# Performance work log

Measured on AMD Instinct MI355X. Metric: run time of the kernel, lower is better.

## Reference

```python
import jax, jax.numpy as jnp
import numpy as np

B, P, M = 2, 2048, 1024
H, D = 16, 64  # num_heads, head_dim; M == H*D

def setup_inputs() -> dict:
    key = jax.random.key(0)
    k1, k2, k3 = jax.random.split(key, 3)
    x = jax.random.normal(k1, (B, P, M), dtype=jnp.float32)
    W_attn = jax.random.normal(k2, (M, 3 * M), dtype=jnp.float32) * 0.02
    b_attn = jnp.zeros((3 * M,), dtype=jnp.float32)
    W_proj = jax.random.normal(k3, (M, M), dtype=jnp.float32) * 0.02
    b_proj = jnp.zeros((M,), dtype=jnp.float32)
    return {"x": x, "W_attn": W_attn, "b_attn": b_attn, "W_proj": W_proj, "b_proj": b_proj}

def reference(x, W_attn, b_attn, W_proj, b_proj):
    b, p, m = x.shape
    # fused QKV projection
    qkv = jnp.einsum('bpm,mn->bpn', x, W_attn) + b_attn  # [b,p,3m]
    q, k, v = jnp.split(qkv, 3, axis=2)
    q = q.reshape(b, p, H, D)
    k = k.reshape(b, p, H, D)
    v = v.reshape(b, p, H, D)
    q = q / jnp.sqrt(jnp.asarray(D, dtype=q.dtype))
    scores = jnp.einsum('bqhd,bkhd->bhqk', q, k)  # [b,h,p,p]
    causal = jnp.tril(jnp.ones((p, p), dtype=bool))  # [p,p]
    big_neg = jnp.finfo(jnp.float32).min
    scores = jnp.where(causal[None, None, :, :], scores, big_neg)
    pattern = jax.nn.softmax(scores, axis=-1)
    z = jnp.einsum('bhqk,bkhd->bqhd', pattern, v)  # [b,p,h,d]
    z = z.reshape(b, p, m)
    out = jnp.einsum('bpm,mn->bpn', z, W_proj) + b_proj
    return out
```

## Files before the change

### kernel.cpp

```cpp
#include <hip/hip_runtime.h>
#include <hip/hip_bf16.h>

typedef __bf16 bf16;
typedef __attribute__((ext_vector_type(8))) __bf16 bf16x8;
typedef __attribute__((ext_vector_type(4))) float f32x4;

#define MFMA16(a, b, c) __builtin_amdgcn_mfma_f32_16x16x32_bf16(a, b, c, 0, 0, 0)
#define GLL16(gp, lp)                                                          \
  __builtin_amdgcn_global_load_lds(                                            \
      (const __attribute__((address_space(1))) void*)(gp),                     \
      (__attribute__((address_space(3))) void*)(lp), 16, 0, 0)

constexpr int Bsz = 2, Pseq = 2048, Mdim = 1024, NH = 16, Dh = 64;
constexpr int ROWS = Bsz * Pseq;
constexpr float LOG2E = 1.4426950408889634f;
constexpr float BIG_NEG = -3.0e38f;
constexpr float M0 = 8.0f;

__global__ __launch_bounds__(256) void k_pre(const float* __restrict__ X,
                                             bf16* __restrict__ Xb,
                                             const float* __restrict__ Wa,
                                             bf16* __restrict__ Wat,
                                             const float* __restrict__ Wp,
                                             bf16* __restrict__ Wpt) {
  __shared__ __align__(16) bf16 tile[64][72];
  int blk = blockIdx.x;
  int t = threadIdx.x;
  if (blk < 1024) {
    const f32x4* X4 = (const f32x4*)X;
    int i0 = blk * 1024 + t;
#pragma unroll
    for (int c = 0; c < 4; ++c) {
      int i = i0 + c * 256;
      f32x4 v = X4[i];
      union { bf16 h[4]; uint2 u; } pk;
      pk.h[0] = (bf16)v[0]; pk.h[1] = (bf16)v[1];
      pk.h[2] = (bf16)v[2]; pk.h[3] = (bf16)v[3];
      ((uint2*)Xb)[i] = pk.u;
    }
    return;
  }
  const float* W; bf16* Wt; int Ndim, n0, k0;
  if (blk < 1792) {
    int bx = blk - 1024;
    W = Wa; Wt = Wat; Ndim = 3 * Mdim;
    n0 = (bx % 48) * 64; k0 = (bx / 48) * 64;
  } else {
    int bx = blk - 1792;
    W = Wp; Wt = Wpt; Ndim = Mdim;
    n0 = (bx & 15) * 64; k0 = (bx >> 4) * 64;
  }
  int tc = t & 15, tr = t >> 4;
#pragma unroll
  for (int pass = 0; pass < 4; ++pass) {
    int r = tr + pass * 16;
    f32x4 v = *(const f32x4*)(W + (size_t)(k0 + r) * Ndim + n0 + tc * 4);
#pragma unroll
    for (int i = 0; i < 4; ++i) tile[tc * 4 + i][r] = (bf16)v[i];
  }
  __syncthreads();
#pragma unroll
  for (int pass = 0; pass < 4; ++pass) {
    int n = tr + pass * 16;
    union { bf16 h[4]; uint2 u; } pk;
#pragma unroll
    for (int i = 0; i < 4; ++i) pk.h[i] = tile[n][tc * 4 + i];
    *(uint2*)(Wt + (size_t)(n0 + n) * Mdim + k0 + tc * 4) = pk.u;
  }
}

template <int TM, int TN>
__device__ __forceinline__ void gemm_core(const bf16* __restrict__ A,
                                          const bf16* __restrict__ Bt,
                                          bf16* Ash, bf16* Bsh, int K,
                                          int row0, int col0,
                                          f32x4 (&acc)[TM / 32][TN / 32]) {
  constexpr int MT = TM / 32, NT = TN / 32;
  int tid = threadIdx.x;
  int lane = tid & 63, w = tid >> 6;
  int l15 = lane & 15, g = lane >> 4, l7 = lane & 7, l8 = lane >> 3;
  int wm = w & 1, wn = w >> 1;
  const bf16* Ag = A + (size_t)(row0 + w * 8 + l8) * K + (l7 ^ l8) * 8;
  const bf16* Bg = Bt + (size_t)(col0 + w * 8 + l8) * K + (l7 ^ l8) * 8;
  bf16* Asb = Ash + w * 512;
  bf16* Bsb = Bsh + w * 512;
  for (int k0 = 0; k0 < K; k0 += 64) {
#pragma unroll
    for (int p = 0; p < MT; ++p)
      GLL16(Ag + (size_t)(p * 32) * K + k0, Asb + p * 2048);
#pragma unroll
    for (int p = 0; p < NT; ++p)
      GLL16(Bg + (size_t)(p * 32) * K + k0, Bsb + p * 2048);
    __syncthreads();
#pragma unroll
    for (int ks = 0; ks < 2; ++ks) {
      int swz = ((ks * 4 + g) ^ l7) * 8;
      bf16x8 af[MT], bfr[NT];
#pragma unroll
      for (int mt = 0; mt < MT; ++mt)
        af[mt] = *(const bf16x8*)(Ash + (wm * (TM / 2) + mt * 16 + l15) * 64 + swz);
#pragma unroll
      for (int nt = 0; nt < NT; ++nt)
        bfr[nt] = *(const bf16x8*)(Bsh + (wn * (TN / 2) + nt * 16 + l15) * 64 + swz);
#pragma unroll
      for (int mt = 0; mt < MT; ++mt)
#pragma unroll
        for (int nt = 0; nt < NT; ++nt)
          acc[mt][nt] = MFMA16(af[mt], bfr[nt], acc[mt][nt]);
    }
    __syncthreads();
  }
}

__global__ __launch_bounds__(512) void k_qkv(const bf16* __restrict__ Xb,
                                             const bf16* __restrict__ Wt,
                                             const float* __restrict__ bias,
                                             bf16* __restrict__ Qo,
                                             bf16* __restrict__ Ko,
                                             bf16* __restrict__ Vto) {
  __shared__ __align__(16) bf16 Ash[128 * 64], Bsh[128 * 64];
  int cb = blockIdx.x, rb = blockIdx.y;
  int row0 = rb * 128, col0 = cb * 128;
  int tid = threadIdx.x;
  int lane = tid & 63, w = tid >> 6;
  int l15 = lane & 15, g = lane >> 4, l7 = lane & 7;
  int wm = w & 1, wn = w >> 1;
  int sr = tid >> 3;
  int sc = (tid & 7) ^ (sr & 7);
  const bf16* Ag = Xb + (size_t)(row0 + sr) * Mdim + sc * 8;
  const bf16* Bg = Wt + (size_t)(col0 + sr) * Mdim + sc * 8;

  f32x4 acc[4][2];
  const f32x4 zero = {0.f, 0.f, 0.f, 0.f};
#pragma unroll
  for (int mt = 0; mt < 4; ++mt)
#pragma unroll
    for (int nt = 0; nt < 2; ++nt) acc[mt][nt] = zero;

  for (int k0 = 0; k0 < Mdim; k0 += 64) {
    GLL16(Ag + k0, Ash + tid * 8);
    GLL16(Ag + (size_t)64 * Mdim + k0, Ash + 4096 + tid * 8);
    GLL16(Bg + k0, Bsh + tid * 8);
    GLL16(Bg + (size_t)64 * Mdim + k0, Bsh + 4096 + tid * 8);
    __syncthreads();
#pragma unroll
    for (int ks = 0; ks < 2; ++ks) {
      int swz = ((ks * 4 + g) ^ l7) * 8;
      bf16x8 af[4], bfr[2];
#pragma unroll
      for (int mt = 0; mt < 4; ++mt)
        af[mt] = *(const bf16x8*)(Ash + (wm * 64 + mt * 16 + l15) * 64 + swz);
#pragma unroll
      for (int nt = 0; nt < 2; ++nt)
        bfr[nt] = *(const bf16x8*)(Bsh + (wn * 32 + nt * 16 + l15) * 64 + swz);
#pragma unroll
      for (int mt = 0; mt < 4; ++mt)
#pragma unroll
        for (int nt = 0; nt < 2; ++nt)
          acc[mt][nt] = MFMA16(af[mt], bfr[nt], acc[mt][nt]);
    }
    __syncthreads();
  }

  int sec = cb >> 3;
  if (sec < 2) {
    bf16* out = sec == 0 ? Qo : Ko;
    float scale = sec == 0 ? (0.125f * LOG2E) : 1.0f;
#pragma unroll
    for (int nt = 0; nt < 2; ++nt) {
      int col = col0 + wn * 32 + nt * 16 + l15;
      int cm = col & 1023;
      int h = cm >> 6, d = cm & 63;
      float bv = bias[col];
#pragma unroll
      for (int mt = 0; mt < 4; ++mt)
#pragma unroll
        for (int r = 0; r < 4; ++r) {
          int row = row0 + wm * 64 + mt * 16 + g * 4 + r;
          int b = row >> 11, p = row & 2047;
          out[(size_t)((b * NH + h) * Pseq + p) * Dh + d] =
              (bf16)((acc[mt][nt][r] + bv) * scale);
        }
    }
  } else {
#pragma unroll
    for (int nt = 0; nt < 2; ++nt) {
      int col = col0 + wn * 32 + nt * 16 + l15;
      int cm = col & 1023;
      int h = cm >> 6, d = cm & 63;
      float bv = bias[col];
#pragma unroll
      for (int mt = 0; mt < 4; ++mt) {
        int row = row0 + wm * 64 + mt * 16 + g * 4;
        int b = row >> 11, p = row & 2047;
        union { bf16 hh[4]; uint2 u; } pk;
#pragma unroll
        for (int r = 0; r < 4; ++r) pk.hh[r] = (bf16)(acc[mt][nt][r] + bv);
        *(uint2*)(Vto + ((size_t)((b * NH + h) * Dh + d)) * Pseq + p) = pk.u;
      }
    }
  }
}

__global__ __launch_bounds__(256, 4) void k_attn(const bf16* __restrict__ Q,
                                                 const bf16* __restrict__ K,
                                                 const bf16* __restrict__ Vt,
                                                 bf16* __restrict__ Z) {
  __shared__ __align__(16) bf16 Ksh[2 * 64 * 64];
  __shared__ __align__(16) bf16 Vsh[2 * 64 * 64];
  __shared__ __align__(16) bf16 Pb[4 * 16 * 64];
  int bh = blockIdx.x;
  int y = blockIdx.y;
  int qt = (y < 16) ? y : 47 - y;
  int b = bh >> 4, h = bh & 15;
  const bf16* Qb = Q + (size_t)bh * Pseq * Dh;
  const bf16* Kb = K + (size_t)bh * Pseq * Dh;
  const bf16* Vb = Vt + (size_t)bh * Dh * Pseq;
  int tid = threadIdx.x;
  int lane = tid & 63, w = tid >> 6;
  int l15 = lane & 15, g = lane >> 4, l7 = lane & 7;
  int q0 = qt * 64;
  int njt = qt + 1;

  bf16x8 qf[2];
#pragma unroll
  for (int ks = 0; ks < 2; ++ks)
    qf[ks] = *(const bf16x8*)(Qb + (size_t)(q0 + w * 16 + l15) * Dh + ks * 32 + g * 8);

  f32x4 O[4];
  const f32x4 zero = {0.f, 0.f, 0.f, 0.f};
#pragma unroll
  for (int nt = 0; nt < 4; ++nt) O[nt] = zero;
  float lacc[4] = {0.f, 0.f, 0.f, 0.f};

  int srow = tid >> 3;
  int sgr = (tid & 7) ^ (srow & 7);
  const bf16* Kgs = Kb + (size_t)srow * Dh + sgr * 8;
  const bf16* Vgs = Vb + (size_t)srow * Pseq + sgr * 8;
  bf16* Pw = Pb + w * 1024;
  int pwr[4], prd[2];
#pragma unroll
  for (int mtl = 0; mtl < 4; ++mtl)
    pwr[mtl] = l15 * 64 + (((mtl * 2 + (g >> 1)) ^ l7) * 8) + (g & 1) * 4;
#pragma unroll
  for (int kl = 0; kl < 2; ++kl)
    prd[kl] = l15 * 64 + (((kl * 4 + g) ^ l7) * 8);

#pragma unroll
  for (int p = 0; p < 2; ++p) {
    GLL16(Kgs + (size_t)(p * 32) * Dh, Ksh + p * 2048 + tid * 8);
    GLL16(Vgs + (size_t)(p * 32) * Pseq, Vsh + p * 2048 + tid * 8);
  }

  for (int j = 0; j < njt; ++j) {
    int buf = j & 1;
    __syncthreads();
    if (j + 1 < njt) {
      const bf16* Kg2 = Kgs + (size_t)((j + 1) * 64) * Dh;
      const bf16* Vg2 = Vgs + (j + 1) * 64;
      bf16* kd = Ksh + (buf ^ 1) * 4096 + tid * 8;
      bf16* vd = Vsh + (buf ^ 1) * 4096 + tid * 8;
#pragma unroll
      for (int p = 0; p < 2; ++p) {
        GLL16(Kg2 + (size_t)(p * 32) * Dh, kd + p * 2048);
        GLL16(Vg2 + (size_t)(p * 32) * Pseq, vd + p * 2048);
      }
    }
    f32x4 S[4];
#pragma unroll
    for (int mt = 0; mt < 4; ++mt) S[mt] = zero;
    const bf16* Kr = Ksh + buf * 4096;
    const bf16* Vr = Vsh + buf * 4096;
#pragma unroll
    for (int ks = 0; ks < 2; ++ks) {
      int swz = ((ks * 4 + g) ^ l7) * 8;
#pragma unroll
      for (int mt = 0; mt < 4; ++mt) {
        bf16x8 kf = *(const bf16x8*)(Kr + (mt * 16 + l15) * 64 + swz);
        S[mt] = MFMA16(kf, qf[ks], S[mt]);
      }
    }
    if (j == njt - 1) {
      int q = q0 + w * 16 + l15;
#pragma unroll
      for (int mt = 0; mt < 4; ++mt) {
        int kvb = j * 64 + mt * 16 + g * 4;
#pragma unroll
        for (int r = 0; r < 4; ++r)
          if (kvb + r > q) S[mt][r] = BIG_NEG;
      }
    }
#pragma unroll
    for (int mt = 0; mt < 4; ++mt) {
      union { bf16 hh[4]; uint2 u; } pk;
#pragma unroll
      for (int r = 0; r < 4; ++r) {
        float p = __builtin_amdgcn_exp2f(S[mt][r] - M0);
        lacc[r] += p;
        pk.hh[r] = (bf16)p;
      }
      *(uint2*)(Pw + pwr[mt]) = pk.u;
    }
#pragma unroll
    for (int kl = 0; kl < 2; ++kl) {
      bf16x8 pf = *(const bf16x8*)(Pw + prd[kl]);
      int swz = ((kl * 4 + g) ^ l7) * 8;
#pragma unroll
      for (int nt = 0; nt < 4; ++nt) {
        bf16x8 vf = *(const bf16x8*)(Vr + (nt * 16 + l15) * 64 + swz);
        O[nt] = MFMA16(pf, vf, O[nt]);
      }
    }
  }
  float l_i = (lacc[0] + lacc[1]) + (lacc[2] + lacc[3]);
  l_i += __shfl_xor(l_i, 16);
  l_i += __shfl_xor(l_i, 32);
#pragma unroll
  for (int r = 0; r < 4; ++r) {
    float li = __shfl(l_i, g * 4 + r);
    float inv = 1.0f / li;
    int q = q0 + w * 16 + g * 4 + r;
    size_t base = ((size_t)(b * Pseq + q)) * Mdim + h * Dh;
#pragma unroll
    for (int nt = 0; nt < 4; ++nt)
      Z[base + nt * 16 + l15] = (bf16)(O[nt][r] * inv);
  }
}

__global__ __launch_bounds__(256) void k_proj(const bf16* __restrict__ Zb,
                                              const bf16* __restrict__ Wt,
                                              const float* __restrict__ bias,
                                              float* __restrict__ Out) {
  __shared__ __align__(16) bf16 Ash[64 * 64], Bsh[64 * 64];
  int cb = blockIdx.x, rb = blockIdx.y;
  int row0 = rb * 64, col0 = cb * 64;
  f32x4 acc[2][2];
  const f32x4 zero = {0.f, 0.f, 0.f, 0.f};
#pragma unroll
  for (int mt = 0; mt < 2; ++mt)
#pragma unroll
    for (int nt = 0; nt < 2; ++nt) acc[mt][nt] = zero;
  gemm_core<64, 64>(Zb, Wt, Ash, Bsh, Mdim, row0, col0, acc);

  int lane = threadIdx.x & 63, w = threadIdx.x >> 6;
  int l15 = lane & 15, g = lane >> 4;
  int wm = w & 1, wn = w >> 1;
#pragma unroll
  for (int nt = 0; nt < 2; ++nt) {
    int col = col0 + wn * 32 + nt * 16 + l15;
    float bv = bias[col];
#pragma unroll
    for (int mt = 0; mt < 2; ++mt)
#pragma unroll
      for (int r = 0; r < 4; ++r) {
        int row = row0 + wm * 32 + mt * 16 + g * 4 + r;
        Out[(size_t)row * Mdim + col] = acc[mt][nt][r] + bv;
      }
  }
}

extern "C" void kernel_launch(void* const* d_in, const int* in_sizes, int n_in,
                              void* d_out, int out_size, void* d_ws, size_t ws_size,
                              hipStream_t stream) {
  const float* x = (const float*)d_in[0];
  const float* W_attn = (const float*)d_in[1];
  const float* b_attn = (const float*)d_in[2];
  const float* W_proj = (const float*)d_in[3];
  const float* b_proj = (const float*)d_in[4];
  float* out = (float*)d_out;

  bf16* Xb = (bf16*)d_ws;
  bf16* Wat = Xb + (size_t)ROWS * Mdim;
  bf16* Wpt = Wat + (size_t)3 * Mdim * Mdim;
  bf16* Qs = Wpt + (size_t)Mdim * Mdim;
  bf16* Ks = Qs + (size_t)ROWS * Mdim;
  bf16* Vts = Ks + (size_t)ROWS * Mdim;
  bf16* Zb = Vts + (size_t)ROWS * Mdim;

  k_pre<<<2048, 256, 0, stream>>>(x, Xb, W_attn, Wat, W_proj, Wpt);
  k_qkv<<<dim3(3 * Mdim / 128, ROWS / 128), 512, 0, stream>>>(Xb, Wat, b_attn, Qs, Ks, Vts);
  k_attn<<<dim3(Bsz * NH, Pseq / 64), 256, 0, stream>>>(Qs, Ks, Vts, Zb);
  k_proj<<<dim3(Mdim / 64, ROWS / 64), 256, 0, stream>>>(Zb, Wpt, b_proj, out);
}
```

Measured before the change: 170.3 us.

## Enlarge attention query tile to 128 and projection row tile to 128

The attention kernel now processes 128 query rows per block: each wave handles two 16-row query subtiles, reusing every K/V tile loaded into shared memory across twice as many queries. The causal mask is applied on the last two KV tiles. The output projection GEMM tile grows from 64x64 to 128x64. This halves global and shared K/V traffic per query and the number of blocks, but doubles per-wave registers (occupancy hint lowered to 2) and leaves fewer blocks for load balancing.

```diff
diff --git a/kernel.cpp b/kernel.cpp
--- a/kernel.cpp
+++ b/kernel.cpp
@@ -202,16 +202,16 @@
   }
 }
 
-__global__ __launch_bounds__(256, 4) void k_attn(const bf16* __restrict__ Q,
+__global__ __launch_bounds__(256, 2) void k_attn(const bf16* __restrict__ Q,
                                                  const bf16* __restrict__ K,
                                                  const bf16* __restrict__ Vt,
                                                  bf16* __restrict__ Z) {
   __shared__ __align__(16) bf16 Ksh[2 * 64 * 64];
   __shared__ __align__(16) bf16 Vsh[2 * 64 * 64];
-  __shared__ __align__(16) bf16 Pb[4 * 16 * 64];
+  __shared__ __align__(16) bf16 Pb[4 * 32 * 64];
   int bh = blockIdx.x;
   int y = blockIdx.y;
-  int qt = (y < 16) ? y : 47 - y;
+  int qt = (y < 8) ? y : 23 - y;
   int b = bh >> 4, h = bh & 15;
   const bf16* Qb = Q + (size_t)bh * Pseq * Dh;
   const bf16* Kb = K + (size_t)bh * Pseq * Dh;
@@ -219,25 +219,30 @@
   int tid = threadIdx.x;
   int lane = tid & 63, w = tid >> 6;
   int l15 = lane & 15, g = lane >> 4, l7 = lane & 7;
-  int q0 = qt * 64;
-  int njt = qt + 1;
-
-  bf16x8 qf[2];
+  int q0 = qt * 128;
+  int njt = 2 * qt + 2;
+
+  bf16x8 qf[2][2];
 #pragma unroll
   for (int ks = 0; ks < 2; ++ks)
-    qf[ks] = *(const bf16x8*)(Qb + (size_t)(q0 + w * 16 + l15) * Dh + ks * 32 + g * 8);
-
-  f32x4 O[4];
+#pragma unroll
+    for (int qn = 0; qn < 2; ++qn)
+      qf[ks][qn] = *(const bf16x8*)(Qb + (size_t)(q0 + w * 32 + qn * 16 + l15) * Dh +
+                                    ks * 32 + g * 8);
+
+  f32x4 O[4][2];
   const f32x4 zero = {0.f, 0.f, 0.f, 0.f};
 #pragma unroll
-  for (int nt = 0; nt < 4; ++nt) O[nt] = zero;
-  float lacc[4] = {0.f, 0.f, 0.f, 0.f};
+  for (int nt = 0; nt < 4; ++nt)
+#pragma unroll
+    for (int qn = 0; qn < 2; ++qn) O[nt][qn] = zero;
+  float lacc[2][4] = {{0.f, 0.f, 0.f, 0.f}, {0.f, 0.f, 0.f, 0.f}};
 
   int srow = tid >> 3;
   int sgr = (tid & 7) ^ (srow & 7);
   const bf16* Kgs = Kb + (size_t)srow * Dh + sgr * 8;
   const bf16* Vgs = Vb + (size_t)srow * Pseq + sgr * 8;
-  bf16* Pw = Pb + w * 1024;
+  bf16* Pw = Pb + w * 2048;
   int pwr[4], prd[2];
 #pragma unroll
   for (int mtl = 0; mtl < 4; ++mtl)
@@ -266,9 +271,11 @@
         GLL16(Vg2 + (size_t)(p * 32) * Pseq, vd + p * 2048);
       }
     }
-    f32x4 S[4];
-#pragma unroll
-    for (int mt = 0; mt < 4; ++mt) S[mt] = zero;
+    f32x4 S[4][2];
+#pragma unroll
+    for (int mt = 0; mt < 4; ++mt)
+#pragma unroll
+      for (int qn = 0; qn < 2; ++qn) S[mt][qn] = zero;
     const bf16* Kr = Ksh + buf * 4096;
     const bf16* Vr = Vsh + buf * 4096;
 #pragma unroll
@@ -277,53 +284,64 @@
 #pragma unroll
       for (int mt = 0; mt < 4; ++mt) {
         bf16x8 kf = *(const bf16x8*)(Kr + (mt * 16 + l15) * 64 + swz);
-        S[mt] = MFMA16(kf, qf[ks], S[mt]);
-      }
-    }
-    if (j == njt - 1) {
-      int q = q0 + w * 16 + l15;
+        S[mt][0] = MFMA16(kf, qf[ks][0], S[mt][0]);
+        S[mt][1] = MFMA16(kf, qf[ks][1], S[mt][1]);
+      }
+    }
+    if (j >= njt - 2) {
+#pragma unroll
+      for (int qn = 0; qn < 2; ++qn) {
+        int q = q0 + w * 32 + qn * 16 + l15;
+#pragma unroll
+        for (int mt = 0; mt < 4; ++mt) {
+          int kvb = j * 64 + mt * 16 + g * 4;
+#pragma unroll
+          for (int r = 0; r < 4; ++r)
+            if (kvb + r > q) S[mt][qn][r] = BIG_NEG;
+        }
+      }
+    }
+#pragma unroll
+    for (int qn = 0; qn < 2; ++qn)
 #pragma unroll
       for (int mt = 0; mt < 4; ++mt) {
-        int kvb = j * 64 + mt * 16 + g * 4;
-#pragma unroll
-        for (int r = 0; r < 4; ++r)
-          if (kvb + r > q) S[mt][r] = BIG_NEG;
-      }
-    }
-#pragma unroll
-    for (int mt = 0; mt < 4; ++mt) {
-      union { bf16 hh[4]; uint2 u; } pk;
-#pragma unroll
-      for (int r = 0; r < 4; ++r) {
-        float p = __builtin_amdgcn_exp2f(S[mt][r] - M0);
-        lacc[r] += p;
-        pk.hh[r] = (bf16)p;
-      }
-      *(uint2*)(Pw + pwr[mt]) = pk.u;
-    }
+        union { bf16 hh[4]; uint2 u; } pk;
+#pragma unroll
+        for (int r = 0; r < 4; ++r) {
+          float p = __builtin_amdgcn_exp2f(S[mt][qn][r] - M0);
+          lacc[qn][r] += p;
+          pk.hh[r] = (bf16)p;
+        }
+        *(uint2*)(Pw + qn * 1024 + pwr[mt]) = pk.u;
+      }
 #pragma unroll
     for (int kl = 0; kl < 2; ++kl) {
-      bf16x8 pf = *(const bf16x8*)(Pw + prd[kl]);
       int swz = ((kl * 4 + g) ^ l7) * 8;
+      bf16x8 pf0 = *(const bf16x8*)(Pw + prd[kl]);
+      bf16x8 pf1 = *(const bf16x8*)(Pw + 1024 + prd[kl]);
 #pragma unroll
       for (int nt = 0; nt < 4; ++nt) {
         bf16x8 vf = *(const bf16x8*)(Vr + (nt * 16 + l15) * 64 + swz);
-        O[nt] = MFMA16(pf, vf, O[nt]);
-      }
-    }
-  }
-  float l_i = (lacc[0] + lacc[1]) + (lacc[2] + lacc[3]);
-  l_i += __shfl_xor(l_i, 16);
-  l_i += __shfl_xor(l_i, 32);
-#pragma unroll
-  for (int r = 0; r < 4; ++r) {
-    float li = __shfl(l_i, g * 4 + r);
-    float inv = 1.0f / li;
-    int q = q0 + w * 16 + g * 4 + r;
-    size_t base = ((size_t)(b * Pseq + q)) * Mdim + h * Dh;
-#pragma unroll
-    for (int nt = 0; nt < 4; ++nt)
-      Z[base + nt * 16 + l15] = (bf16)(O[nt][r] * inv);
+        O[nt][0] = MFMA16(pf0, vf, O[nt][0]);
+        O[nt][1] = MFMA16(pf1, vf, O[nt][1]);
+      }
+    }
+  }
+#pragma unroll
+  for (int qn = 0; qn < 2; ++qn) {
+    float l_i = (lacc[qn][0] + lacc[qn][1]) + (lacc[qn][2] + lacc[qn][3]);
+    l_i += __shfl_xor(l_i, 16);
+    l_i += __shfl_xor(l_i, 32);
+#pragma unroll
+    for (int r = 0; r < 4; ++r) {
+      float li = __shfl(l_i, g * 4 + r);
+      float inv = 1.0f / li;
+      int q = q0 + w * 32 + qn * 16 + g * 4 + r;
+      size_t base = ((size_t)(b * Pseq + q)) * Mdim + h * Dh;
+#pragma unroll
+      for (int nt = 0; nt < 4; ++nt)
+        Z[base + nt * 16 + l15] = (bf16)(O[nt][qn][r] * inv);
+    }
   }
 }
 
@@ -331,16 +349,16 @@
                                               const bf16* __restrict__ Wt,
                                               const float* __restrict__ bias,
                                               float* __restrict__ Out) {
-  __shared__ __align__(16) bf16 Ash[64 * 64], Bsh[64 * 64];
+  __shared__ __align__(16) bf16 Ash[128 * 64], Bsh[64 * 64];
   int cb = blockIdx.x, rb = blockIdx.y;
-  int row0 = rb * 64, col0 = cb * 64;
-  f32x4 acc[2][2];
+  int row0 = rb * 128, col0 = cb * 64;
+  f32x4 acc[4][2];
   const f32x4 zero = {0.f, 0.f, 0.f, 0.f};
 #pragma unroll
-  for (int mt = 0; mt < 2; ++mt)
+  for (int mt = 0; mt < 4; ++mt)
 #pragma unroll
     for (int nt = 0; nt < 2; ++nt) acc[mt][nt] = zero;
-  gemm_core<64, 64>(Zb, Wt, Ash, Bsh, Mdim, row0, col0, acc);
+  gemm_core<128, 64>(Zb, Wt, Ash, Bsh, Mdim, row0, col0, acc);
 
   int lane = threadIdx.x & 63, w = threadIdx.x >> 6;
   int l15 = lane & 15, g = lane >> 4;
@@ -350,10 +368,10 @@
     int col = col0 + wn * 32 + nt * 16 + l15;
     float bv = bias[col];
 #pragma unroll
-    for (int mt = 0; mt < 2; ++mt)
+    for (int mt = 0; mt < 4; ++mt)
 #pragma unroll
       for (int r = 0; r < 4; ++r) {
-        int row = row0 + wm * 32 + mt * 16 + g * 4 + r;
+        int row = row0 + wm * 64 + mt * 16 + g * 4 + r;
         Out[(size_t)row * Mdim + col] = acc[mt][nt][r] + bv;
       }
   }
@@ -379,6 +397,6 @@
 
   k_pre<<<2048, 256, 0, stream>>>(x, Xb, W_attn, Wat, W_proj, Wpt);
   k_qkv<<<dim3(3 * Mdim / 128, ROWS / 128), 512, 0, stream>>>(Xb, Wat, b_attn, Qs, Ks, Vts);
-  k_attn<<<dim3(Bsz * NH, Pseq / 64), 256, 0, stream>>>(Qs, Ks, Vts, Zb);
-  k_proj<<<dim3(Mdim / 64, ROWS / 64), 256, 0, stream>>>(Zb, Wpt, b_proj, out);
-}
+  k_attn<<<dim3(Bsz * NH, Pseq / 128), 256, 0, stream>>>(Qs, Ks, Vts, Zb);
+  k_proj<<<dim3(Mdim / 64, ROWS / 128), 256, 0, stream>>>(Zb, Wpt, b_proj, out);
+}
```

Result: slower. 180.0 us (+5.7%).
